# Performance work log

Hardware: AMD Instinct MI355X
Metric: run time of the kernel (lower is better)

The kernel has to match this reference:

```python
import jax, jax.numpy as jnp
import numpy as np

N, F, C, H, D = 32768, 128, 4, 8, 32
DM = H * D  # 256, d_model
E, B = 65536, 8192


def _pe():
    # sinusoidal positional encoding over the chain dimension, shape [C, DM]
    pos = jnp.arange(C, dtype=jnp.float32)[:, None]
    di = jnp.arange(0, DM, 2, dtype=jnp.float32)[None, :]
    div = 10000.0 ** (di / DM)
    pe = jnp.zeros((C, DM), jnp.float32)
    pe = pe.at[:, 0::2].set(jnp.sin(pos / div))
    pe = pe.at[:, 1::2].set(jnp.cos(pos / div))
    return pe


def _leaky(v):
    return jnp.where(v >= 0, v, 0.2 * v)


def setup_inputs() -> dict:
    key = jax.random.key(0)
    ks = jax.random.split(key, 6)
    x = jax.random.normal(ks[0], (N, F), jnp.float32)
    edge_index = jax.random.randint(ks[1], (2, E), 0, N)
    bridge_index = jax.random.randint(ks[2], (2, B), 0, N)
    W_in = jax.random.normal(ks[3], (DM, F), jnp.float32) * 0.05       # linear_input.weight
    double_attn = jax.random.normal(ks[4], (1, C * H, D), jnp.float32) * 0.1
    W_res = jax.random.normal(ks[5], (C * DM, F), jnp.float32) * 0.05  # residual_linear.weight
    bias = jnp.zeros((C * DM,), jnp.float32)
    prelu_w = jnp.float32(0.25)  # nn.PReLU default
    return {"x": x, "edge_index": edge_index, "bridge_index": bridge_index,
            "W_in": W_in, "double_attn": double_attn, "W_res": W_res,
            "bias": bias, "prelu_w": prelu_w}


def reference(x, edge_index, bridge_index, W_in, double_attn, W_res, bias, prelu_w):
    n = x.shape[0]
    # project + chain positional encoding -> [n, C, H, D]
    xl = x @ W_in.T                                   # [n, DM]
    xr = (xl[:, None, :] + _pe()[None]).reshape(n, C, H, D)

    src_bond, dst_bond = edge_index[0], edge_index[1]
    bond_attn = _leaky(xr[src_bond] + xr[dst_bond])   # [E, C, H, D]

    src_bridge, dst_bridge = bridge_index[0], bridge_index[1]
    ch = jnp.arange(C)
    prev_ch = jnp.clip(ch - 1, 0, None)
    next_ch = jnp.clip(ch + 1, None, C - 1)
    src2dst = _leaky(xr[dst_bridge] + xr[src_bridge][:, next_ch]).at[:, -1].set(0.0)
    dst2src = _leaky(xr[src_bridge] + xr[dst_bridge][:, prev_ch]).at[:, 0].set(0.0)

    full_src = jnp.concatenate([src_bond, src_bridge, dst_bridge])   # [Et]
    full_dst = jnp.concatenate([dst_bond, dst_bridge, src_bridge])   # [Et]
    x_src = jnp.concatenate([xr[src_bond], xr[src_bridge], xr[dst_bridge]], axis=0).reshape(-1, C * H, D)
    edge_attn = jnp.concatenate([bond_attn, src2dst, dst2src], axis=0).reshape(-1, C * H, D)

    scores = (double_attn * edge_attn).sum(-1)        # [Et, C*H]
    exp_s = jnp.exp(scores - scores.max())            # global-max stabilized, as in original
    denom = jax.ops.segment_sum(exp_s, full_dst, num_segments=n)     # [n, C*H]
    alpha = exp_s / (denom[full_dst] + 1e-16)

    # NOTE: faithful to original bug - x_src (per-edge, len Et) indexed by NODE ids
    proj = x_src[full_src] * alpha[..., None]         # [Et, C*H, D]
    out = jax.ops.segment_sum(proj, full_dst, num_segments=n)        # [n, C*H, D]

    out = out + (x @ W_res.T).reshape(n, C * H, D)    # residual
    out = out.reshape(n, C * H * D) + bias            # concat + bias
    out = jnp.where(out >= 0, out, prelu_w * out)     # PReLU
    return out
```

## Files before the change

kernel.cpp:

```cpp
#include <hip/hip_runtime.h>
#include <math.h>

#define N_NODES 32768
#define F_IN    128
#define C_CH    4
#define H_HEADS 8
#define D_DIM   32
#define DM      256
#define E_BOND  65536
#define B_BRIDGE 8192
#define ET      (E_BOND + 2*B_BRIDGE)
#define OUTC    1024
#define CAP     24
#define NCOLS   1280

#define WS_XL      0u
#define WS_PE      33554432u
#define WS_SCORES  33558528u
#define WS_BUCKET2 44044288u
#define WS_CNT     50335744u
#define WS_GMAX    50466816u
#define WS_RESID   50470912u
#define WS_XB      117579776u
#define WS_WC      125968384u

typedef __attribute__((ext_vector_type(8))) short bf16x8;
typedef __attribute__((ext_vector_type(4))) float f32x4;
typedef __attribute__((ext_vector_type(4))) _Float16 f16x4;

__device__ __forceinline__ unsigned enc_f32(float f) {
    unsigned u = __float_as_uint(f);
    return (u & 0x80000000u) ? ~u : (u | 0x80000000u);
}
__device__ __forceinline__ float dec_f32(unsigned u) {
    return (u & 0x80000000u) ? __uint_as_float(u & 0x7fffffffu) : __uint_as_float(~u);
}
__device__ __forceinline__ float leaky(float v) { return v >= 0.f ? v : 0.2f*v; }
__device__ __forceinline__ ushort f2bf(float f) {
    unsigned u = __float_as_uint(f);
    unsigned r = (u + 0x7fffu + ((u >> 16) & 1u)) >> 16;
    return (ushort)r;
}

__global__ void pe_init_kernel(float* __restrict__ pe, unsigned* __restrict__ gmax) {
    int tid = threadIdx.x;
    int c = tid >> 8, p = tid & 255;
    float expo = (float)(p & ~1) * (1.0f/256.0f);
    float div  = powf(10000.0f, expo);
    float arg  = (float)c / div;
    pe[tid] = (p & 1) ? cosf(arg) : sinf(arg);
    if (tid == 0) *gmax = 0u;
}

__global__ __launch_bounds__(256) void cvt_x_kernel(const float* __restrict__ x,
                                                    ushort* __restrict__ xb) {
    const long i = (long)blockIdx.x*256 + threadIdx.x;
    float4 v = ((const float4*)x)[i];
    ushort4 o; o.x = f2bf(v.x); o.y = f2bf(v.y); o.z = f2bf(v.z); o.w = f2bf(v.w);
    ((ushort4*)xb)[i] = o;
}
__global__ __launch_bounds__(256) void cvt_w_kernel(const float* __restrict__ W_in,
                                                    const float* __restrict__ W_res,
                                                    ushort* __restrict__ wc) {
    const int i = blockIdx.x*256 + threadIdx.x;
    float4 v = (i < 8192) ? ((const float4*)W_in)[i] : ((const float4*)W_res)[i - 8192];
    ushort4 o; o.x = f2bf(v.x); o.y = f2bf(v.y); o.z = f2bf(v.z); o.w = f2bf(v.w);
    ((ushort4*)wc)[i] = o;
}

#define LDSK 72
__global__ __launch_bounds__(256) void mfma_gemm(
        const ushort* __restrict__ xb, const ushort* __restrict__ wc,
        float* __restrict__ xl, _Float16* __restrict__ resid) {
    __shared__ ushort As[128*LDSK];
    __shared__ ushort Bs[128*LDSK];
    const int tid = threadIdx.x;
    const int m0 = blockIdx.x * 128;
    const int n0 = blockIdx.y * 128;
    const int lane = tid & 63, wv = tid >> 6;
    const int wm = wv & 1, wn = wv >> 1;
    const int quad = lane >> 4, l15 = lane & 15;
    const int mbase = wm*64, nbase = wn*64;
    f32x4 acc[4][4] = {};

    for (int kt = 0; kt < 2; ++kt) {
        if (kt) __syncthreads();
#pragma unroll
        for (int i = 0; i < 4; ++i) {
            int c = tid + i*256;
            int row = c >> 3, seg = c & 7;
            *(uint4*)&As[row*LDSK + seg*8] =
                *(const uint4*)(xb + (long)(m0 + row)*F_IN + kt*64 + seg*8);
        }
#pragma unroll
        for (int i = 0; i < 4; ++i) {
            int c = tid + i*256;
            int row = c >> 3, seg = c & 7;
            *(uint4*)&Bs[row*LDSK + seg*8] =
                *(const uint4*)(wc + (long)(n0 + row)*F_IN + kt*64 + seg*8);
        }
        __syncthreads();
#pragma unroll
        for (int ks = 0; ks < 2; ++ks) {
            const int ko = ks*32 + quad*8;
            bf16x8 af[4], bfr[4];
#pragma unroll
            for (int mi = 0; mi < 4; ++mi)
                af[mi] = *(const bf16x8*)&As[(mbase + mi*16 + l15)*LDSK + ko];
#pragma unroll
            for (int ni = 0; ni < 4; ++ni)
                bfr[ni] = *(const bf16x8*)&Bs[(nbase + ni*16 + l15)*LDSK + ko];
#pragma unroll
            for (int mi = 0; mi < 4; ++mi)
#pragma unroll
                for (int ni = 0; ni < 4; ++ni)
                    acc[mi][ni] = __builtin_amdgcn_mfma_f32_16x16x32_bf16(
                        af[mi], bfr[ni], acc[mi][ni], 0, 0, 0);
        }
    }

    if (n0 < DM) {
#pragma unroll
        for (int mi = 0; mi < 4; ++mi) {
            const int mrow = m0 + mbase + mi*16 + quad*4;
#pragma unroll
            for (int ni = 0; ni < 4; ++ni) {
                const int col = n0 + nbase + ni*16 + l15;
#pragma unroll
                for (int r = 0; r < 4; ++r)
                    xl[(long)(mrow + r)*DM + col] = acc[mi][ni][r];
            }
        }
    } else {
        const int coloff = n0 - DM;
#pragma unroll
        for (int mi = 0; mi < 4; ++mi) {
            const int mrow = m0 + mbase + mi*16 + quad*4;
#pragma unroll
            for (int ni = 0; ni < 4; ++ni) {
                const int col = coloff + nbase + ni*16 + l15;
#pragma unroll
                for (int r = 0; r < 4; ++r)
                    resid[(long)(mrow + r)*OUTC + col] = (_Float16)acc[mi][ni][r];
            }
        }
    }
}

__global__ __launch_bounds__(256) void scores_kernel(
        const float* __restrict__ xl, const float* __restrict__ pe,
        const int* __restrict__ ei, const int* __restrict__ bi,
        const float* __restrict__ datt, float* __restrict__ scores,
        unsigned* __restrict__ gmax, int* __restrict__ counts,
        int2* __restrict__ bucket2) {
    const int tid = threadIdx.x;
    const int l = tid & 63, wv = tid >> 6;
    const int pos = l * 4;
    const int h = l >> 3, dq = l & 7;

    float4 pe4[4], w4[4];
#pragma unroll
    for (int c = 0; c < 4; ++c) {
        pe4[c] = *(const float4*)(pe + c*DM + pos);
        w4[c]  = *(const float4*)(datt + (c*H_HEADS + h)*D_DIM + dq*4);
    }

    float wmax = -1e30f;
    const int stride = gridDim.x * 4;
    for (int e = blockIdx.x*4 + wv; e < ET; e += stride) {
        int nA, nB, type;
        if (e < E_BOND) {
            nA = ei[e]; nB = ei[E_BOND + e]; type = 0;
        } else if (e < E_BOND + B_BRIDGE) {
            int i = e - E_BOND;
            nA = bi[B_BRIDGE + i]; nB = bi[i]; type = 1;
        } else {
            int i = e - E_BOND - B_BRIDGE;
            nA = bi[i]; nB = bi[B_BRIDGE + i]; type = 2;
        }

        if (l == 0) {
            int dst = (type == 0) ? nB : nA;
            int fs  = (type == 0) ? nA : nB;
            int g   = ei[fs];
            int slot = atomicAdd(&counts[dst], 1);
            if (slot < CAP) bucket2[dst*CAP + slot] = make_int2(e, g);
        }

        float4 a = *(const float4*)(xl + (long)nA*DM + pos);
        float4 b = *(const float4*)(xl + (long)nB*DM + pos);
        float4 s = make_float4(a.x + b.x, a.y + b.y, a.z + b.z, a.w + b.w);

        float p[4];
#pragma unroll
        for (int c = 0; c < 4; ++c) {
            int cB = (type == 0) ? c : (type == 1 ? (c+1 < 3 ? c+1 : 3)
                                                  : (c-1 > 0 ? c-1 : 0));
            bool z = (type == 1 && c == 3) || (type == 2 && c == 0);
            float4 pa = pe4[c];
            float4 pb = (cB == 0) ? pe4[0] : (cB == 1) ? pe4[1]
                       : (cB == 2) ? pe4[2] : pe4[3];
            float v0 = leaky(s.x + pa.x + pb.x);
            float v1 = leaky(s.y + pa.y + pb.y);
            float v2 = leaky(s.z + pa.z + pb.z);
            float v3 = leaky(s.w + pa.w + pb.w);
            float d = w4[c].x*v0 + w4[c].y*v1 + w4[c].z*v2 + w4[c].w*v3;
            p[c] = z ? 0.f : d;
            p[c] += __shfl_xor(p[c], 1);
            p[c] += __shfl_xor(p[c], 2);
            p[c] += __shfl_xor(p[c], 4);
        }
        float val = (dq == 0) ? p[0] : (dq == 1) ? p[1] : (dq == 2) ? p[2] : p[3];
        if (dq < 4) scores[(long)e*32 + dq*8 + h] = val;
        wmax = fmaxf(wmax, fmaxf(fmaxf(p[0], p[1]), fmaxf(p[2], p[3])));
    }

    wmax = fmaxf(wmax, __shfl_xor(wmax, 8));
    wmax = fmaxf(wmax, __shfl_xor(wmax, 16));
    wmax = fmaxf(wmax, __shfl_xor(wmax, 32));
    __shared__ float sm[4];
    if (l == 0) sm[wv] = wmax;
    __syncthreads();
    if (tid == 0) {
        float mm = fmaxf(fmaxf(sm[0], sm[1]), fmaxf(sm[2], sm[3]));
        atomicMax(gmax, enc_f32(mm));
    }
}

__global__ __launch_bounds__(256) void alpha_kernel(
        const int* __restrict__ counts, const int2* __restrict__ bucket2,
        const unsigned* __restrict__ gmax, float* __restrict__ scores) {
    const int t = threadIdx.x;
    const int n = blockIdx.x*8 + (t >> 5);
    const int ch = t & 31;
    const float m = dec_f32(*gmax);
    const int cnt = min(counts[n], CAP);

    float ex[CAP];
    float den = 0.f;
#pragma unroll
    for (int i = 0; i < CAP; ++i) {
        if (i < cnt) {
            int e = bucket2[n*CAP + i].x;
            float v = __expf(scores[(long)e*32 + ch] - m);
            ex[i] = v; den += v;
        }
    }
    const float inv = 1.f / (den + 1e-16f);
#pragma unroll
    for (int i = 0; i < CAP; ++i) {
        if (i < cnt) {
            int e = bucket2[n*CAP + i].x;
            scores[(long)e*32 + ch] = ex[i] * inv;
        }
    }
}

__global__ __launch_bounds__(256) void gather_kernel(
        const float* __restrict__ xl, const float* __restrict__ pe,
        const float* __restrict__ alpha, const int* __restrict__ counts,
        const int2* __restrict__ bucket2, const _Float16* __restrict__ resid,
        const float* __restrict__ bias, const float* __restrict__ pw,
        float* __restrict__ out) {
    const int n = blockIdx.x;
    const int t = threadIdx.x;
    const int ch = t >> 3;
    const int d0 = (t & 7) * 4;
    const int h = ch & 7, c = ch >> 3;
    const int cnt = min(counts[n], CAP);
    const int col = ch*D_DIM + d0;

    const float4 pv = *(const float4*)(pe + c*DM + h*D_DIM + d0);
    float4 acc = make_float4(0.f, 0.f, 0.f, 0.f);
    float asum = 0.f;

    for (int i = 0; i < cnt; ++i) {
        int2 eg = bucket2[n*CAP + i];
        float a = alpha[(long)eg.x*32 + ch];
        float4 xv = *(const float4*)(xl + (long)eg.y*DM + h*D_DIM + d0);
        acc.x += a*xv.x; acc.y += a*xv.y; acc.z += a*xv.z; acc.w += a*xv.w;
        asum += a;
    }
    acc.x += asum*pv.x; acc.y += asum*pv.y; acc.z += asum*pv.z; acc.w += asum*pv.w;

    const f16x4 hv = *(const f16x4*)(resid + (long)n*OUTC + col);
    const float4 b = *(const float4*)(bias + col);
    const float w = *pw;
    float r0 = acc.x + (float)hv.x + b.x;
    float r1 = acc.y + (float)hv.y + b.y;
    float r2 = acc.z + (float)hv.z + b.z;
    float r3 = acc.w + (float)hv.w + b.w;
    r0 = r0 >= 0.f ? r0 : w*r0;
    r1 = r1 >= 0.f ? r1 : w*r1;
    r2 = r2 >= 0.f ? r2 : w*r2;
    r3 = r3 >= 0.f ? r3 : w*r3;
    *(float4*)(out + (long)n*OUTC + col) = make_float4(r0, r1, r2, r3);
}

extern "C" void kernel_launch(void* const* d_in, const int* in_sizes, int n_in,
                              void* d_out, int out_size, void* d_ws, size_t ws_size,
                              hipStream_t stream) {
    const float* x     = (const float*)d_in[0];
    const int*   ei    = (const int*)d_in[1];
    const int*   bi    = (const int*)d_in[2];
    const float* W_in  = (const float*)d_in[3];
    const float* datt  = (const float*)d_in[4];
    const float* W_res = (const float*)d_in[5];
    const float* bias  = (const float*)d_in[6];
    const float* pw    = (const float*)d_in[7];
    float* out = (float*)d_out;
    char*  ws  = (char*)d_ws;

    float*     xl      = (float*)(ws + WS_XL);
    float*     pe      = (float*)(ws + WS_PE);
    float*     scores  = (float*)(ws + WS_SCORES);
    int2*      bucket2 = (int2*)(ws + WS_BUCKET2);
    int*       counts  = (int*)(ws + WS_CNT);
    unsigned*  gmax    = (unsigned*)(ws + WS_GMAX);
    _Float16*  resid   = (_Float16*)(ws + WS_RESID);
    ushort*    xb      = (ushort*)(ws + WS_XB);
    ushort*    wc      = (ushort*)(ws + WS_WC);

    hipMemsetAsync(counts, 0, (size_t)N_NODES*4, stream);
    pe_init_kernel<<<1, 1024, 0, stream>>>(pe, gmax);
    cvt_x_kernel<<<(N_NODES*F_IN/4)/256, 256, 0, stream>>>(x, xb);
    cvt_w_kernel<<<(NCOLS*F_IN/4 + 255)/256, 256, 0, stream>>>(W_in, W_res, wc);
    {
        dim3 grid(N_NODES/128, NCOLS/128);
        mfma_gemm<<<grid, 256, 0, stream>>>(xb, wc, xl, resid);
    }
    scores_kernel<<<2560, 256, 0, stream>>>(xl, pe, ei, bi, datt, scores, gmax,
                                            counts, bucket2);
    alpha_kernel<<<N_NODES/8, 256, 0, stream>>>(counts, bucket2, gmax, scores);
    gather_kernel<<<N_NODES, 256, 0, stream>>>(xl, pe, scores, counts, bucket2,
                                               resid, bias, pw, out);
}
```

Measured before the change: 338.2 us.

## Split bucket build into own kernel, use bf16 node features for scores, unroll gather

Moves the per-destination bucket construction out of the scores kernel into a separate one-thread-per-edge kernel. The GEMM now also emits a bf16 copy of the projected features. The scores kernel reads this bf16 copy and processes 8 edges per wave with batched independent loads, cutting gather bytes and exposing memory-level parallelism. The gather loop is unrolled by four with predicated tails so loads can be issued ahead. The cost is an extra 16MB bf16 write in the GEMM, an extra launch, and reduced precision in the attention scores.

```diff
diff --git a/kernel.cpp b/kernel.cpp
--- a/kernel.cpp
+++ b/kernel.cpp
@@ -15,14 +15,15 @@
 #define NCOLS   1280
 
 #define WS_XL      0u
-#define WS_PE      33554432u
-#define WS_SCORES  33558528u
-#define WS_BUCKET2 44044288u
-#define WS_CNT     50335744u
-#define WS_GMAX    50466816u
-#define WS_RESID   50470912u
-#define WS_XB      117579776u
-#define WS_WC      125968384u
+#define WS_XLB     33554432u
+#define WS_PE      50331648u
+#define WS_SCORES  50335744u
+#define WS_BUCKET2 60821504u
+#define WS_CNT     67112960u
+#define WS_GMAX    67244032u
+#define WS_RESID   67248128u
+#define WS_XB      134356992u
+#define WS_WC      142745600u
 
 typedef __attribute__((ext_vector_type(8))) short bf16x8;
 typedef __attribute__((ext_vector_type(4))) float f32x4;
@@ -40,6 +41,19 @@
     unsigned u = __float_as_uint(f);
     unsigned r = (u + 0x7fffu + ((u >> 16) & 1u)) >> 16;
     return (ushort)r;
+}
+__device__ __forceinline__ float bf2f(ushort u) {
+    return __uint_as_float((unsigned)u << 16);
+}
+
+__device__ __forceinline__ void edge_decode(int e, const int* __restrict__ ei,
+                                            const int* __restrict__ bi,
+                                            int& nA, int& nB, int& tp) {
+    if (e < E_BOND)               { nA = ei[e]; nB = ei[E_BOND + e]; tp = 0; }
+    else if (e < E_BOND+B_BRIDGE) { int i = e - E_BOND;
+                                    nA = bi[B_BRIDGE + i]; nB = bi[i]; tp = 1; }
+    else                          { int i = e - E_BOND - B_BRIDGE;
+                                    nA = bi[i]; nB = bi[B_BRIDGE + i]; tp = 2; }
 }
 
 __global__ void pe_init_kernel(float* __restrict__ pe, unsigned* __restrict__ gmax) {
@@ -71,7 +85,8 @@
 #define LDSK 72
 __global__ __launch_bounds__(256) void mfma_gemm(
         const ushort* __restrict__ xb, const ushort* __restrict__ wc,
-        float* __restrict__ xl, _Float16* __restrict__ resid) {
+        float* __restrict__ xl, ushort* __restrict__ xlb,
+        _Float16* __restrict__ resid) {
     __shared__ ushort As[128*LDSK];
     __shared__ ushort Bs[128*LDSK];
     const int tid = threadIdx.x;
@@ -127,8 +142,11 @@
             for (int ni = 0; ni < 4; ++ni) {
                 const int col = n0 + nbase + ni*16 + l15;
 #pragma unroll
-                for (int r = 0; r < 4; ++r)
-                    xl[(long)(mrow + r)*DM + col] = acc[mi][ni][r];
+                for (int r = 0; r < 4; ++r) {
+                    float v = acc[mi][ni][r];
+                    xl [(long)(mrow + r)*DM + col] = v;
+                    xlb[(long)(mrow + r)*DM + col] = f2bf(v);
+                }
             }
         }
     } else {
@@ -147,12 +165,25 @@
     }
 }
 
+__global__ __launch_bounds__(256) void build_kernel(
+        const int* __restrict__ ei, const int* __restrict__ bi,
+        int* __restrict__ counts, int2* __restrict__ bucket2) {
+    const int e = blockIdx.x*256 + threadIdx.x;
+    if (e >= ET) return;
+    int nA, nB, tp;
+    edge_decode(e, ei, bi, nA, nB, tp);
+    const int dst = (tp == 0) ? nB : nA;
+    const int fs  = (tp == 0) ? nA : nB;
+    const int g   = ei[fs];
+    int slot = atomicAdd(&counts[dst], 1);
+    if (slot < CAP) bucket2[dst*CAP + slot] = make_int2(e, g);
+}
+
 __global__ __launch_bounds__(256) void scores_kernel(
-        const float* __restrict__ xl, const float* __restrict__ pe,
+        const ushort* __restrict__ xlb, const float* __restrict__ pe,
         const int* __restrict__ ei, const int* __restrict__ bi,
         const float* __restrict__ datt, float* __restrict__ scores,
-        unsigned* __restrict__ gmax, int* __restrict__ counts,
-        int2* __restrict__ bucket2) {
+        unsigned* __restrict__ gmax) {
     const int tid = threadIdx.x;
     const int l = tid & 63, wv = tid >> 6;
     const int pos = l * 4;
@@ -166,53 +197,51 @@
     }
 
     float wmax = -1e30f;
-    const int stride = gridDim.x * 4;
-    for (int e = blockIdx.x*4 + wv; e < ET; e += stride) {
-        int nA, nB, type;
-        if (e < E_BOND) {
-            nA = ei[e]; nB = ei[E_BOND + e]; type = 0;
-        } else if (e < E_BOND + B_BRIDGE) {
-            int i = e - E_BOND;
-            nA = bi[B_BRIDGE + i]; nB = bi[i]; type = 1;
-        } else {
-            int i = e - E_BOND - B_BRIDGE;
-            nA = bi[i]; nB = bi[B_BRIDGE + i]; type = 2;
-        }
-
-        if (l == 0) {
-            int dst = (type == 0) ? nB : nA;
-            int fs  = (type == 0) ? nA : nB;
-            int g   = ei[fs];
-            int slot = atomicAdd(&counts[dst], 1);
-            if (slot < CAP) bucket2[dst*CAP + slot] = make_int2(e, g);
-        }
-
-        float4 a = *(const float4*)(xl + (long)nA*DM + pos);
-        float4 b = *(const float4*)(xl + (long)nB*DM + pos);
-        float4 s = make_float4(a.x + b.x, a.y + b.y, a.z + b.z, a.w + b.w);
-
-        float p[4];
-#pragma unroll
-        for (int c = 0; c < 4; ++c) {
-            int cB = (type == 0) ? c : (type == 1 ? (c+1 < 3 ? c+1 : 3)
-                                                  : (c-1 > 0 ? c-1 : 0));
-            bool z = (type == 1 && c == 3) || (type == 2 && c == 0);
-            float4 pa = pe4[c];
-            float4 pb = (cB == 0) ? pe4[0] : (cB == 1) ? pe4[1]
-                       : (cB == 2) ? pe4[2] : pe4[3];
-            float v0 = leaky(s.x + pa.x + pb.x);
-            float v1 = leaky(s.y + pa.y + pb.y);
-            float v2 = leaky(s.z + pa.z + pb.z);
-            float v3 = leaky(s.w + pa.w + pb.w);
-            float d = w4[c].x*v0 + w4[c].y*v1 + w4[c].z*v2 + w4[c].w*v3;
-            p[c] = z ? 0.f : d;
-            p[c] += __shfl_xor(p[c], 1);
-            p[c] += __shfl_xor(p[c], 2);
-            p[c] += __shfl_xor(p[c], 4);
-        }
-        float val = (dq == 0) ? p[0] : (dq == 1) ? p[1] : (dq == 2) ? p[2] : p[3];
-        if (dq < 4) scores[(long)e*32 + dq*8 + h] = val;
-        wmax = fmaxf(wmax, fmaxf(fmaxf(p[0], p[1]), fmaxf(p[2], p[3])));
+    const int wavebase = (blockIdx.x*4 + wv) * 8;
+#pragma unroll
+    for (int gdx = 0; gdx < 2; ++gdx) {
+        const int e0 = wavebase + gdx*4;
+        int nA[4], nB[4], tp[4];
+#pragma unroll
+        for (int j = 0; j < 4; ++j)
+            edge_decode(e0 + j, ei, bi, nA[j], nB[j], tp[j]);
+        ushort4 ua[4], ub[4];
+#pragma unroll
+        for (int j = 0; j < 4; ++j) {
+            ua[j] = *(const ushort4*)(xlb + (long)nA[j]*DM + pos);
+            ub[j] = *(const ushort4*)(xlb + (long)nB[j]*DM + pos);
+        }
+#pragma unroll
+        for (int j = 0; j < 4; ++j) {
+            const int e = e0 + j, t = tp[j];
+            float sx = bf2f(ua[j].x) + bf2f(ub[j].x);
+            float sy = bf2f(ua[j].y) + bf2f(ub[j].y);
+            float sz = bf2f(ua[j].z) + bf2f(ub[j].z);
+            float sw = bf2f(ua[j].w) + bf2f(ub[j].w);
+
+            float p[4];
+#pragma unroll
+            for (int c = 0; c < 4; ++c) {
+                int cB = (t == 0) ? c : (t == 1 ? (c+1 < 3 ? c+1 : 3)
+                                               : (c-1 > 0 ? c-1 : 0));
+                bool z = (t == 1 && c == 3) || (t == 2 && c == 0);
+                float4 pa = pe4[c];
+                float4 pb = (cB == 0) ? pe4[0] : (cB == 1) ? pe4[1]
+                           : (cB == 2) ? pe4[2] : pe4[3];
+                float v0 = leaky(sx + pa.x + pb.x);
+                float v1 = leaky(sy + pa.y + pb.y);
+                float v2 = leaky(sz + pa.z + pb.z);
+                float v3 = leaky(sw + pa.w + pb.w);
+                float d = w4[c].x*v0 + w4[c].y*v1 + w4[c].z*v2 + w4[c].w*v3;
+                p[c] = z ? 0.f : d;
+                p[c] += __shfl_xor(p[c], 1);
+                p[c] += __shfl_xor(p[c], 2);
+                p[c] += __shfl_xor(p[c], 4);
+            }
+            float val = (dq == 0) ? p[0] : (dq == 1) ? p[1] : (dq == 2) ? p[2] : p[3];
+            if (dq < 4) scores[(long)e*32 + dq*8 + h] = val;
+            wmax = fmaxf(wmax, fmaxf(fmaxf(p[0], p[1]), fmaxf(p[2], p[3])));
+        }
     }
 
     wmax = fmaxf(wmax, __shfl_xor(wmax, 8));
@@ -269,23 +298,30 @@
     const int h = ch & 7, c = ch >> 3;
     const int cnt = min(counts[n], CAP);
     const int col = ch*D_DIM + d0;
-
-    const float4 pv = *(const float4*)(pe + c*DM + h*D_DIM + d0);
-    float4 acc = make_float4(0.f, 0.f, 0.f, 0.f);
-    float asum = 0.f;
-
-    for (int i = 0; i < cnt; ++i) {
-        int2 eg = bucket2[n*CAP + i];
-        float a = alpha[(long)eg.x*32 + ch];
-        float4 xv = *(const float4*)(xl + (long)eg.y*DM + h*D_DIM + d0);
-        acc.x += a*xv.x; acc.y += a*xv.y; acc.z += a*xv.z; acc.w += a*xv.w;
-        asum += a;
-    }
-    acc.x += asum*pv.x; acc.y += asum*pv.y; acc.z += asum*pv.z; acc.w += asum*pv.w;
+    const int nb = n*CAP;
 
     const f16x4 hv = *(const f16x4*)(resid + (long)n*OUTC + col);
     const float4 b = *(const float4*)(bias + col);
     const float w = *pw;
+    const float4 pv = *(const float4*)(pe + c*DM + h*D_DIM + d0);
+
+    float4 acc = make_float4(0.f, 0.f, 0.f, 0.f);
+    float asum = 0.f;
+
+    for (int i0 = 0; i0 < cnt; i0 += 4) {
+#pragma unroll
+        for (int j = 0; j < 4; ++j) {
+            const int idx = i0 + j;
+            const int safe = idx < cnt ? idx : i0;
+            int2 eg = bucket2[nb + safe];
+            float a = (idx < cnt) ? alpha[(long)eg.x*32 + ch] : 0.f;
+            float4 xv = *(const float4*)(xl + (long)eg.y*DM + h*D_DIM + d0);
+            acc.x += a*xv.x; acc.y += a*xv.y; acc.z += a*xv.z; acc.w += a*xv.w;
+            asum += a;
+        }
+    }
+    acc.x += asum*pv.x; acc.y += asum*pv.y; acc.z += asum*pv.z; acc.w += asum*pv.w;
+
     float r0 = acc.x + (float)hv.x + b.x;
     float r1 = acc.y + (float)hv.y + b.y;
     float r2 = acc.z + (float)hv.z + b.z;
@@ -312,6 +348,7 @@
     char*  ws  = (char*)d_ws;
 
     float*     xl      = (float*)(ws + WS_XL);
+    ushort*    xlb     = (ushort*)(ws + WS_XLB);
     float*     pe      = (float*)(ws + WS_PE);
     float*     scores  = (float*)(ws + WS_SCORES);
     int2*      bucket2 = (int2*)(ws + WS_BUCKET2);
@@ -325,12 +362,12 @@
     pe_init_kernel<<<1, 1024, 0, stream>>>(pe, gmax);
     cvt_x_kernel<<<(N_NODES*F_IN/4)/256, 256, 0, stream>>>(x, xb);
     cvt_w_kernel<<<(NCOLS*F_IN/4 + 255)/256, 256, 0, stream>>>(W_in, W_res, wc);
+    build_kernel<<<(ET+255)/256, 256, 0, stream>>>(ei, bi, counts, bucket2);
     {
         dim3 grid(N_NODES/128, NCOLS/128);
-        mfma_gemm<<<grid, 256, 0, stream>>>(xb, wc, xl, resid);
-    }
-    scores_kernel<<<2560, 256, 0, stream>>>(xl, pe, ei, bi, datt, scores, gmax,
-                                            counts, bucket2);
+        mfma_gemm<<<grid, 256, 0, stream>>>(xb, wc, xl, xlb, resid);
+    }
+    scores_kernel<<<2560, 256, 0, stream>>>(xlb, pe, ei, bi, datt, scores, gmax);
     alpha_kernel<<<N_NODES/8, 256, 0, stream>>>(counts, bucket2, gmax, scores);
     gather_kernel<<<N_NODES, 256, 0, stream>>>(xl, pe, scores, counts, bucket2,
                                                resid, bias, pw, out);
```

Result: slower. 345.6 us (+2.2%).
